# Optimization experiments

Measured on AMD Instinct MI355X. Metric: run time of the kernel, lower is better.

Reference implementation:

```python
import jax, jax.numpy as jnp
import numpy as np

B, C, T = 128, 272, 1024
D1, K = 270, 32


def setup_inputs() -> dict:
    key = jax.random.key(0)
    k1, k2, k3, k4 = jax.random.split(key, 4)
    X = jax.random.normal(k1, (B, C, T), dtype=jnp.float32)
    loc = jax.random.uniform(k2, (C, 2), dtype=jnp.float32)  # 2D sensor coords in [0,1]
    z_re = jax.random.normal(k3, (D1, K, K), dtype=jnp.float32)
    z_im = jax.random.normal(k4, (D1, K, K), dtype=jnp.float32)
    return {"X": X, "loc": loc, "z_re": z_re, "z_im": z_im}


def reference(X, loc, z_re, z_im):
    # X: [B, C, T]; loc: [C, 2]; z_re/z_im: [D1, K, K]
    Kdim = z_re.shape[1]
    x, y = loc[:, 0], loc[:, 1]                      # [C]
    k = jnp.arange(Kdim, dtype=X.dtype)
    # phase[k, l, c] = 2*pi*(k*x[c] + l*y[c])
    phase = 2.0 * jnp.pi * (k[:, None, None] * x[None, None, :]
                            + k[None, :, None] * y[None, None, :])  # [K, K, C]
    # a[j, c] = sum_{k,l} z_re[j,k,l]*cos(phase) + z_im[j,k,l]*sin(phase)
    A = (jnp.einsum('dkl,klc->dc', z_re, jnp.cos(phase))
         + jnp.einsum('dkl,klc->dc', z_im, jnp.sin(phase)))  # [D1, C]
    # exp(a_j) / sum_c exp(a_j) == softmax over channels (same math)
    w = jax.nn.softmax(A, axis=1)                    # [D1, C]
    # out[b, j, t] = sum_c w[j,c] * X[b,c,t]
    return jnp.einsum('dc,bct->bdt', w, X)           # [B, D1, T]
```

## Files before the change

kernel.cpp:

```cpp
#include <hip/hip_runtime.h>

#define BB 128
#define CC 272
#define TT 1024
#define DD 270
#define KK 32
#define NKC 9
#define MP 272
#define NT 256
#define WCH (CC * KK)
#define WBYTES (NKC * WCH * 2)

typedef __attribute__((ext_vector_type(8))) short s16x8;
typedef __attribute__((ext_vector_type(4))) float f32x4;

__device__ __forceinline__ unsigned short f2bf(float f) {
  unsigned int u = __builtin_bit_cast(unsigned int, f);
  u += 0x7fffu + ((u >> 16) & 1u);
  return (unsigned short)(u >> 16);
}

__global__ __launch_bounds__(288) void phaseA_kernel(
    const float* __restrict__ loc, const float* __restrict__ z_re,
    const float* __restrict__ z_im, float* __restrict__ A) {
  const int d = blockIdx.x;
  const int p = blockIdx.y;
  const int c = threadIdx.x;
  if (c >= CC) return;
  const float TWO_PI = 6.28318530717958647692f;
  float x = loc[2 * c], y = loc[2 * c + 1];
  float sx, cx, sy, cyv;
  sincosf(TWO_PI * x, &sx, &cx);
  sincosf(TWO_PI * y, &sy, &cyv);
  float cl[KK], sl[KK];
  cl[0] = 1.f; sl[0] = 0.f;
#pragma unroll
  for (int l = 1; l < KK; ++l) {
    cl[l] = cl[l - 1] * cyv - sl[l - 1] * sy;
    sl[l] = sl[l - 1] * cyv + cl[l - 1] * sy;
  }
  const int k0 = p * 8;
  float sk, ck;
  sincosf(TWO_PI * (float)k0 * x, &sk, &ck);
  const float* zr = z_re + (size_t)d * (KK * KK) + k0 * KK;
  const float* zi = z_im + (size_t)d * (KK * KK) + k0 * KK;
  float acc = 0.f;
  for (int k = 0; k < 8; ++k) {
    float s_rc = 0.f, s_rs = 0.f, s_ic = 0.f, s_is = 0.f;
#pragma unroll
    for (int l = 0; l < KK; ++l) {
      float vr = zr[k * KK + l];
      float vi = zi[k * KK + l];
      s_rc += vr * cl[l];
      s_rs += vr * sl[l];
      s_ic += vi * cl[l];
      s_is += vi * sl[l];
    }
    acc += ck * (s_rc + s_is) + sk * (s_ic - s_rs);
    float nck = ck * cx - sk * sx;
    sk = sk * cx + ck * sx;
    ck = nck;
  }
  atomicAdd(&A[d * CC + c], acc);
}

__global__ __launch_bounds__(64) void softmax_kernel(
    const float* __restrict__ A, unsigned short* __restrict__ wb) {
  const int d = blockIdx.x;
  const int lane = threadIdx.x;
  const bool live = (d < DD);
  float v[5];
  float inv = 0.f;
  if (live) {
    float m = -3.0e38f;
#pragma unroll
    for (int j = 0; j < 5; ++j) {
      int cidx = lane + 64 * j;
      v[j] = (cidx < CC) ? A[(size_t)d * CC + cidx] : -3.0e38f;
      m = fmaxf(m, v[j]);
    }
#pragma unroll
    for (int off = 32; off >= 1; off >>= 1) m = fmaxf(m, __shfl_xor(m, off, 64));
    float s = 0.f;
#pragma unroll
    for (int j = 0; j < 5; ++j) {
      int cidx = lane + 64 * j;
      v[j] = (cidx < CC) ? expf(v[j] - m) : 0.f;
      s += v[j];
    }
#pragma unroll
    for (int off = 32; off >= 1; off >>= 1) s += __shfl_xor(s, off, 64);
    inv = 1.f / s;
  }
#pragma unroll
  for (int j = 0; j < 5; ++j) {
    int kk = lane + 64 * j;
    if (kk < NKC * KK) {
      unsigned short val = 0;
      if (live && kk < CC) val = f2bf(v[j] * inv);
      int kc = kk >> 5, ks = kk & 31, s = ks >> 3, o = ks & 7;
      wb[(size_t)kc * WCH + d * KK + ((s ^ (d & 3)) << 3) + o] = val;
    }
  }
}

__global__ __launch_bounds__(1024) void gemm_kernel(
    const float* __restrict__ X, const unsigned short* __restrict__ wb,
    float* __restrict__ out) {
  __shared__ unsigned short wlds[NKC * WCH];
  const int bid = blockIdx.x;
  const int b = bid >> 2;
  const int t0 = (bid & 3) * NT;
  const int tid = threadIdx.x;
  const int lane = tid & 63;
  const int wv = tid >> 6;
  const int q = lane >> 4;
  const int r16 = lane & 15;

  {
    const char* src = (const char*)wb;
    char* dst = (char*)wlds;
#pragma unroll
    for (int r = 0; r < 10; ++r) {
      int idx = tid + r * 1024;
      if (idx < WBYTES / 16) {
        __builtin_amdgcn_global_load_lds(
            (const __attribute__((address_space(1))) unsigned int*)(src + idx * 16),
            (__attribute__((address_space(3))) unsigned int*)(dst + idx * 16),
            16, 0, 0);
      }
    }
  }

  f32x4 acc[17];
#pragma unroll
  for (int i = 0; i < 17; ++i) acc[i] = (f32x4){0.f, 0.f, 0.f, 0.f};

  const float* Xb = X + (size_t)b * (CC * TT) + t0 + wv * 16 + r16;
  const int csub = q * 8;
  const int base_l = r16 * 64 + ((q ^ (r16 & 3)) << 4);

  float xf[8];
#pragma unroll
  for (int j = 0; j < 8; ++j) xf[j] = Xb[(size_t)(csub + j) * TT];

  __syncthreads();

  for (int kc = 0; kc < NKC; ++kc) {
    float xn[8];
    if (kc < NKC - 1) {
      const int cbase = (kc + 1) * KK + csub;
#pragma unroll
      for (int j = 0; j < 8; ++j)
        xn[j] = (cbase + j < CC) ? Xb[(size_t)(cbase + j) * TT] : 0.f;
    } else {
#pragma unroll
      for (int j = 0; j < 8; ++j) xn[j] = 0.f;
    }
    union { unsigned int u[4]; s16x8 v; } bf;
#pragma unroll
    for (int j2 = 0; j2 < 4; ++j2)
      bf.u[j2] = (unsigned int)f2bf(xf[2 * j2]) |
                 ((unsigned int)f2bf(xf[2 * j2 + 1]) << 16);
    const char* wchunk = (const char*)wlds + kc * (WCH * 2);
#pragma unroll
    for (int mt = 0; mt < 17; ++mt) {
      s16x8 afrag = *(const s16x8*)(wchunk + mt * 1024 + base_l);
      acc[mt] = __builtin_amdgcn_mfma_f32_16x16x32_bf16(afrag, bf.v, acc[mt], 0, 0, 0);
    }
#pragma unroll
    for (int j = 0; j < 8; ++j) xf[j] = xn[j];
  }

  float* op = out + (size_t)b * (DD * TT) + t0 + wv * 16 + r16;
#pragma unroll
  for (int mt = 0; mt < 17; ++mt) {
#pragma unroll
    for (int r = 0; r < 4; ++r) {
      int drow = mt * 16 + q * 4 + r;
      if (drow < DD) op[(size_t)drow * TT] = acc[mt][r];
    }
  }
}

extern "C" void kernel_launch(void* const* d_in, const int* in_sizes, int n_in,
                              void* d_out, int out_size, void* d_ws, size_t ws_size,
                              hipStream_t stream) {
  const float* X = (const float*)d_in[0];
  const float* loc = (const float*)d_in[1];
  const float* z_re = (const float*)d_in[2];
  const float* z_im = (const float*)d_in[3];
  float* out = (float*)d_out;

  float* A = (float*)d_ws;
  unsigned short* wbf = (unsigned short*)((char*)d_ws + 294912);

  hipMemsetAsync(A, 0, DD * CC * sizeof(float), stream);
  phaseA_kernel<<<dim3(DD, 4), 288, 0, stream>>>(loc, z_re, z_im, A);
  softmax_kernel<<<MP, 64, 0, stream>>>(A, wbf);
  gemm_kernel<<<BB * (TT / NT), 1024, 0, stream>>>(X, wbf, out);
}
```

Baseline: 314.4 us.

## Drop LDS weight staging; load MFMA-ready weight fragments from global per wave

```diff
diff --git a/kernel.cpp b/kernel.cpp
--- a/kernel.cpp
+++ b/kernel.cpp
@@ -6,10 +6,9 @@
 #define DD 270
 #define KK 32
 #define NKC 9
+#define NMT 17
 #define MP 272
-#define NT 256
-#define WCH (CC * KK)
-#define WBYTES (NKC * WCH * 2)
+#define WBYTES (NKC * NMT * 64 * 16)
 
 typedef __attribute__((ext_vector_type(8))) short s16x8;
 typedef __attribute__((ext_vector_type(4))) float f32x4;
@@ -92,94 +91,111 @@
     for (int off = 32; off >= 1; off >>= 1) s += __shfl_xor(s, off, 64);
     inv = 1.f / s;
   }
+  const int mt = d >> 4, mrow = d & 15;
 #pragma unroll
   for (int j = 0; j < 5; ++j) {
     int kk = lane + 64 * j;
     if (kk < NKC * KK) {
       unsigned short val = 0;
       if (live && kk < CC) val = f2bf(v[j] * inv);
-      int kc = kk >> 5, ks = kk & 31, s = ks >> 3, o = ks & 7;
-      wb[(size_t)kc * WCH + d * KK + ((s ^ (d & 3)) << 3) + o] = val;
-    }
-  }
-}
-
-__global__ __launch_bounds__(1024) void gemm_kernel(
+      int kc = kk >> 5, hi = (kk >> 3) & 3, jj = kk & 7;
+      wb[((size_t)(kc * NMT + mt) << 9) + (((hi << 4) | mrow) << 3) + jj] = val;
+    }
+  }
+}
+
+__global__ __launch_bounds__(256, 2) void gemm_kernel(
     const float* __restrict__ X, const unsigned short* __restrict__ wb,
     float* __restrict__ out) {
-  __shared__ unsigned short wlds[NKC * WCH];
   const int bid = blockIdx.x;
-  const int b = bid >> 2;
-  const int t0 = (bid & 3) * NT;
+  const int b = bid >> 4;
+  const int t0 = (bid & 15) << 6;
   const int tid = threadIdx.x;
   const int lane = tid & 63;
-  const int wv = tid >> 6;
+  const int dw = tid >> 6;
   const int q = lane >> 4;
   const int r16 = lane & 15;
-
-  {
-    const char* src = (const char*)wb;
-    char* dst = (char*)wlds;
-#pragma unroll
-    for (int r = 0; r < 10; ++r) {
-      int idx = tid + r * 1024;
-      if (idx < WBYTES / 16) {
-        __builtin_amdgcn_global_load_lds(
-            (const __attribute__((address_space(1))) unsigned int*)(src + idx * 16),
-            (__attribute__((address_space(3))) unsigned int*)(dst + idx * 16),
-            16, 0, 0);
+  const bool has5 = (dw == 0);
+
+  f32x4 acc[5][4];
+#pragma unroll
+  for (int i = 0; i < 5; ++i)
+#pragma unroll
+    for (int f = 0; f < 4; ++f) acc[i][f] = (f32x4){0.f, 0.f, 0.f, 0.f};
+
+  const unsigned short* wf = wb + (size_t)lane * 8;
+  const float* Xb = X + (size_t)b * (CC * TT) + t0 + r16;
+  const int csub = q << 3;
+
+  s16x8 a_cur[5], a_nxt[5];
+  float xf[32], xn[32];
+
+#pragma unroll
+  for (int i = 0; i < 4; ++i)
+    a_cur[i] = *(const s16x8*)(wf + ((size_t)(dw + (i << 2)) << 9));
+  if (has5) a_cur[4] = *(const s16x8*)(wf + ((size_t)16 << 9));
+#pragma unroll
+  for (int f = 0; f < 4; ++f)
+#pragma unroll
+    for (int j = 0; j < 8; ++j)
+      xf[f * 8 + j] = Xb[(size_t)(csub + j) * TT + (f << 4)];
+
+#pragma unroll
+  for (int kc = 0; kc < NKC; ++kc) {
+    if (kc < NKC - 1) {
+      const int cb = (kc + 1) * KK + csub;
+#pragma unroll
+      for (int i = 0; i < 4; ++i)
+        a_nxt[i] = *(const s16x8*)(wf + ((size_t)((kc + 1) * NMT + dw + (i << 2)) << 9));
+      if (has5)
+        a_nxt[4] = *(const s16x8*)(wf + ((size_t)((kc + 1) * NMT + 16) << 9));
+#pragma unroll
+      for (int f = 0; f < 4; ++f)
+#pragma unroll
+        for (int j = 0; j < 8; ++j)
+          xn[f * 8 + j] = (cb + j < CC) ? Xb[(size_t)(cb + j) * TT + (f << 4)] : 0.f;
+    }
+    union { unsigned int u[4]; s16x8 v; } bf[4];
+#pragma unroll
+    for (int f = 0; f < 4; ++f)
+#pragma unroll
+      for (int p = 0; p < 4; ++p)
+        bf[f].u[p] = (unsigned int)f2bf(xf[f * 8 + 2 * p]) |
+                     ((unsigned int)f2bf(xf[f * 8 + 2 * p + 1]) << 16);
+#pragma unroll
+    for (int i = 0; i < 4; ++i)
+#pragma unroll
+      for (int f = 0; f < 4; ++f)
+        acc[i][f] = __builtin_amdgcn_mfma_f32_16x16x32_bf16(a_cur[i], bf[f].v, acc[i][f], 0, 0, 0);
+    if (has5) {
+#pragma unroll
+      for (int f = 0; f < 4; ++f)
+        acc[4][f] = __builtin_amdgcn_mfma_f32_16x16x32_bf16(a_cur[4], bf[f].v, acc[4][f], 0, 0, 0);
+    }
+#pragma unroll
+    for (int i = 0; i < 5; ++i) a_cur[i] = a_nxt[i];
+#pragma unroll
+    for (int v2 = 0; v2 < 32; ++v2) xf[v2] = xn[v2];
+  }
+
+  float* op = out + (size_t)b * (DD * TT) + t0 + r16;
+#pragma unroll
+  for (int i = 0; i < 4; ++i) {
+    const int mtb = (dw + (i << 2)) << 4;
+#pragma unroll
+    for (int f = 0; f < 4; ++f)
+#pragma unroll
+      for (int r = 0; r < 4; ++r)
+        op[(size_t)(mtb + q * 4 + r) * TT + (f << 4)] = acc[i][f][r];
+  }
+  if (has5) {
+#pragma unroll
+    for (int f = 0; f < 4; ++f)
+#pragma unroll
+      for (int r = 0; r < 4; ++r) {
+        const int drow = 256 + q * 4 + r;
+        if (drow < DD) op[(size_t)drow * TT + (f << 4)] = acc[4][f][r];
       }
-    }
-  }
-
-  f32x4 acc[17];
-#pragma unroll
-  for (int i = 0; i < 17; ++i) acc[i] = (f32x4){0.f, 0.f, 0.f, 0.f};
-
-  const float* Xb = X + (size_t)b * (CC * TT) + t0 + wv * 16 + r16;
-  const int csub = q * 8;
-  const int base_l = r16 * 64 + ((q ^ (r16 & 3)) << 4);
-
-  float xf[8];
-#pragma unroll
-  for (int j = 0; j < 8; ++j) xf[j] = Xb[(size_t)(csub + j) * TT];
-
-  __syncthreads();
-
-  for (int kc = 0; kc < NKC; ++kc) {
-    float xn[8];
-    if (kc < NKC - 1) {
-      const int cbase = (kc + 1) * KK + csub;
-#pragma unroll
-      for (int j = 0; j < 8; ++j)
-        xn[j] = (cbase + j < CC) ? Xb[(size_t)(cbase + j) * TT] : 0.f;
-    } else {
-#pragma unroll
-      for (int j = 0; j < 8; ++j) xn[j] = 0.f;
-    }
-    union { unsigned int u[4]; s16x8 v; } bf;
-#pragma unroll
-    for (int j2 = 0; j2 < 4; ++j2)
-      bf.u[j2] = (unsigned int)f2bf(xf[2 * j2]) |
-                 ((unsigned int)f2bf(xf[2 * j2 + 1]) << 16);
-    const char* wchunk = (const char*)wlds + kc * (WCH * 2);
-#pragma unroll
-    for (int mt = 0; mt < 17; ++mt) {
-      s16x8 afrag = *(const s16x8*)(wchunk + mt * 1024 + base_l);
-      acc[mt] = __builtin_amdgcn_mfma_f32_16x16x32_bf16(afrag, bf.v, acc[mt], 0, 0, 0);
-    }
-#pragma unroll
-    for (int j = 0; j < 8; ++j) xf[j] = xn[j];
-  }
-
-  float* op = out + (size_t)b * (DD * TT) + t0 + wv * 16 + r16;
-#pragma unroll
-  for (int mt = 0; mt < 17; ++mt) {
-#pragma unroll
-    for (int r = 0; r < 4; ++r) {
-      int drow = mt * 16 + q * 4 + r;
-      if (drow < DD) op[(size_t)drow * TT] = acc[mt][r];
-    }
   }
 }
 
@@ -198,5 +214,5 @@
   hipMemsetAsync(A, 0, DD * CC * sizeof(float), stream);
   phaseA_kernel<<<dim3(DD, 4), 288, 0, stream>>>(loc, z_re, z_im, A);
   softmax_kernel<<<MP, 64, 0, stream>>>(A, wbf);
-  gemm_kernel<<<BB * (TT / NT), 1024, 0, stream>>>(X, wbf, out);
-}
+  gemm_kernel<<<BB * (TT / 64), 256, 0, stream>>>(X, wbf, out);
+}
```

Result: slower. 325.2 us (+3.4%).
